# Kernel optimization log

Measured on AMD Instinct MI355X. Metric: run time of the kernel, lower is better.

Reference implementation:

```python
import jax, jax.numpy as jnp
import numpy as np

N_NODES = 20000

def gcn(h, W, b, src, dst):
    # DGL GraphConv, norm='both': D_out^-1/2 on src, aggregate, D_in^-1/2 on dst, then W, b
    E = src.shape[0]
    ones = jnp.ones((E,), dtype=h.dtype)
    out_deg = jnp.clip(jax.ops.segment_sum(ones, src, N_NODES), 1.0)
    in_deg = jnp.clip(jax.ops.segment_sum(ones, dst, N_NODES), 1.0)
    dn_src = jax.lax.rsqrt(out_deg)  # [N]
    dn_dst = jax.lax.rsqrt(in_deg)
    hs = h * dn_src[None, :, None]           # [B,N,H]
    msg = hs[:, src, :]                      # [B,E,H] gather
    agg = jax.vmap(lambda m: jax.ops.segment_sum(m, dst, N_NODES))(msg)  # [B,N,H]
    agg = agg * dn_dst[None, :, None]
    return agg @ W + b

def setup_inputs() -> dict:
    key = jax.random.key(0)
    ks = jax.random.split(key, 16)
    B, N, H, I, E = 4, N_NODES, 128, 64, 320000
    inp = {
        'x': jax.random.normal(ks[0], (B, I), jnp.float32),
        'h_prev': jax.random.normal(ks[1], (B, N, H), jnp.float32),
        'c_prev': jax.random.normal(ks[2], (B, N, H), jnp.float32),
        'src': jax.random.randint(ks[3], (E,), 0, N, jnp.int32),
        'dst': jax.random.randint(ks[4], (E,), 0, N, jnp.int32),
    }
    s_in = 1.0 / np.sqrt(I)
    s_h = 1.0 / np.sqrt(H)
    inp['Wi'] = jax.random.uniform(ks[5], (I, H), jnp.float32, -s_in, s_in)
    inp['bi'] = jax.random.uniform(ks[6], (H,), jnp.float32, -s_in, s_in)
    inp['Wf'] = jax.random.uniform(ks[7], (I, H), jnp.float32, -s_in, s_in)
    inp['bf'] = jax.random.uniform(ks[8], (H,), jnp.float32, -s_in, s_in)
    inp['Wo'] = jax.random.uniform(ks[9], (I, H), jnp.float32, -s_in, s_in)
    inp['bo'] = jax.random.uniform(ks[10], (H,), jnp.float32, -s_in, s_in)
    inp['Wc'] = jax.random.uniform(ks[11], (I, H), jnp.float32, -s_in, s_in)
    inp['bc'] = jax.random.uniform(ks[12], (H,), jnp.float32, -s_in, s_in)
    inp['Wg'] = jax.random.uniform(ks[13], (H, H), jnp.float32, -s_h, s_h)
    inp['bg'] = jax.random.uniform(ks[14], (H,), jnp.float32, -s_h, s_h)
    return inp

def reference(x, h_prev, c_prev, src, dst, Wi, bi, Wf, bf, Wo, bo, Wc, bc, Wg, bg):
    # gcn_h(g, h_prev) is identical in all four gates -> compute once
    gh = gcn(h_prev, Wg, bg, src, dst)  # [B,N,H]
    i_t = jax.nn.sigmoid((x @ Wi + bi)[:, None, :] + gh)
    f_t = jax.nn.sigmoid((x @ Wf + bf)[:, None, :] + gh)
    o_t = jax.nn.sigmoid((x @ Wo + bo)[:, None, :] + gh)
    c_tilde = jnp.tanh((x @ Wc + bc)[:, None, :] + gh)
    c_t = f_t * c_prev + i_t * c_tilde
    h_t = o_t * jnp.tanh(c_t)
    return h_t, c_t
```

## Files before the change

kernel.cpp:

```cpp
#include <hip/hip_runtime.h>
#include <hip/hip_bf16.h>

#define N_NODES 20000
#define B 4
#define H 128
#define I_DIM 64
#define E_MAX 320000
#define CAP 64

typedef __attribute__((ext_vector_type(8))) short short8;
typedef __attribute__((ext_vector_type(4))) float float4v;

__device__ int   g_cnt_dst[N_NODES];
__device__ int   g_deg_src[N_NODES];
__device__ int   g_csr[N_NODES * CAP];
__device__ __align__(16) float g_xg[4 * B * H];
__device__ __align__(16) uint2 g_hs[N_NODES * H];
__device__ __align__(16) unsigned short g_wgB[H * H];

__global__ __launch_bounds__(256)
void degree_kernel(const int* __restrict__ src, int E, int eb,
                   const float* __restrict__ x,
                   const float* __restrict__ Wi, const float* __restrict__ bi,
                   const float* __restrict__ Wf, const float* __restrict__ bf_,
                   const float* __restrict__ Wo, const float* __restrict__ bo,
                   const float* __restrict__ Wc, const float* __restrict__ bc,
                   const float* __restrict__ Wg) {
    int blk = blockIdx.x;
    int t = threadIdx.x;
    if (blk < eb) {
        int e = blk * 256 + t;
        if (e < E) atomicAdd(&g_deg_src[src[e]], 1);
    } else if (blk < eb + 8) {
        int bid = blk - eb;
        int g = bid >> 1;
        int b = ((bid & 1) << 1) | (t >> 7);
        int h = t & 127;
        const float* W;
        const float* bb;
        switch (g) {
            case 0: W = Wi; bb = bi; break;
            case 1: W = Wf; bb = bf_; break;
            case 2: W = Wo; bb = bo; break;
            default: W = Wc; bb = bc; break;
        }
        float acc = bb[h];
#pragma unroll
        for (int i = 0; i < I_DIM; i++)
            acc += x[b * I_DIM + i] * W[i * H + h];
        g_xg[(b * H + h) * 4 + g] = acc;
    } else {
        int i = (blk - eb - 8) * 256 + t;
        int tn = i >> 11;
        int rem = i & 2047;
        int kb = rem >> 9;
        int rem2 = rem & 511;
        int lane = rem2 >> 3;
        int j = rem2 & 7;
        int k  = kb * 32 + (lane >> 4) * 8 + j;
        int nn = tn * 16 + (lane & 15);
        __hip_bfloat16 hv = __float2bfloat16(Wg[k * H + nn]);
        g_wgB[i] = *reinterpret_cast<unsigned short*>(&hv);
    }
}

__global__ __launch_bounds__(256)
void mid_kernel(const float* __restrict__ h_prev,
                const int* __restrict__ src, const int* __restrict__ dst, int E) {
    const int PACK_BLKS = (N_NODES * H) / 256;
    int blk = blockIdx.x;
    int t = threadIdx.x;

    if (blk < PACK_BLKS) {
        int i = blk * 256 + t;
        int n = i >> 7;
        float sc = rsqrtf(fmaxf((float)g_deg_src[n], 1.0f));
        const long stride = (long)N_NODES * H;
        float v0 = h_prev[i] * sc;
        float v1 = h_prev[i + stride] * sc;
        float v2 = h_prev[i + 2 * stride] * sc;
        float v3 = h_prev[i + 3 * stride] * sc;
        __hip_bfloat162 p01 = __float22bfloat162_rn(make_float2(v0, v1));
        __hip_bfloat162 p23 = __float22bfloat162_rn(make_float2(v2, v3));
        uint2 wv;
        wv.x = *reinterpret_cast<unsigned int*>(&p01);
        wv.y = *reinterpret_cast<unsigned int*>(&p23);
        g_hs[i] = wv;
    } else {
        int e = (blk - PACK_BLKS) * 256 + t;
        if (e < E) {
            int d = dst[e];
            int slot = atomicAdd(&g_cnt_dst[d], 1);
            if (slot < CAP) g_csr[(d << 6) + slot] = src[e];
        }
    }
}

__device__ __forceinline__ float fast_sigmoid(float z) {
    return 1.f / (1.f + __expf(-z));
}
__device__ __forceinline__ float fast_tanh(float z) {
    return 1.f - 2.f / (__expf(2.f * z) + 1.f);
}
__device__ __forceinline__ unsigned pack2bf(float lo, float hi) {
    __hip_bfloat162 p = __float22bfloat162_rn(make_float2(lo, hi));
    return *reinterpret_cast<unsigned*>(&p);
}

__global__ __launch_bounds__(256)
void fused_kernel(const float* __restrict__ bg,
                  const float* __restrict__ c_prev,
                  float* __restrict__ out_h, float* __restrict__ out_c) {
    int t = threadIdx.x;
    int w = t >> 6;
    int lane = t & 63;
    int q = (blockIdx.x * 4 + w) * 4;
    const long stride = (long)N_NODES * H;

    __shared__ int            sbase[4][4 * 64];
    __shared__ unsigned short Atile[4][16][136];

    int cnt0 = g_cnt_dst[q + 0];
    int cnt1 = g_cnt_dst[q + 1];
    int cnt2 = g_cnt_dst[q + 2];
    int cnt3 = g_cnt_dst[q + 3];
    float dd0 = rsqrtf(fmaxf((float)cnt0, 1.0f)); if (cnt0 > CAP) cnt0 = CAP;
    float dd1 = rsqrtf(fmaxf((float)cnt1, 1.0f)); if (cnt1 > CAP) cnt1 = CAP;
    float dd2 = rsqrtf(fmaxf((float)cnt2, 1.0f)); if (cnt2 > CAP) cnt2 = CAP;
    float dd3 = rsqrtf(fmaxf((float)cnt3, 1.0f)); if (cnt3 > CAP) cnt3 = CAP;

    {
        int s0 = g_csr[((q + 0) << 6) + (lane < cnt0 ? lane : 0)];
        int s1 = g_csr[((q + 1) << 6) + (lane < cnt1 ? lane : 0)];
        int s2 = g_csr[((q + 2) << 6) + (lane < cnt2 ? lane : 0)];
        int s3 = g_csr[((q + 3) << 6) + (lane < cnt3 ? lane : 0)];
        sbase[w][0 * 64 + lane] = s0 << 6;
        sbase[w][1 * 64 + lane] = s1 << 6;
        sbase[w][2 * 64 + lane] = s2 << 6;
        sbase[w][3 * 64 + lane] = s3 << 6;
    }

    const uint4* hs4 = reinterpret_cast<const uint4*>(g_hs);
    const int* sb = sbase[w];

#define ACCV(v) { \
        __hip_bfloat162 p; float2 f; \
        p = *reinterpret_cast<__hip_bfloat162*>(&(v).x); f = __bfloat1622float2(p); a0 += f.x; a1 += f.y; \
        p = *reinterpret_cast<__hip_bfloat162*>(&(v).y); f = __bfloat1622float2(p); a2 += f.x; a3 += f.y; \
        p = *reinterpret_cast<__hip_bfloat162*>(&(v).z); f = __bfloat1622float2(p); a4 += f.x; a5 += f.y; \
        p = *reinterpret_cast<__hip_bfloat162*>(&(v).w); f = __bfloat1622float2(p); a6 += f.x; a7 += f.y; }

#define GATHER_NODE(i, cnt, dd) { \
        float a0 = 0.f, a1 = 0.f, a2 = 0.f, a3 = 0.f; \
        float a4 = 0.f, a5 = 0.f, a6 = 0.f, a7 = 0.f; \
        int j = 0; \
        for (; j + 16 <= (cnt); j += 16) { \
            int b0 = sb[(i) * 64 + j];      int b1 = sb[(i) * 64 + j + 1]; \
            int b2 = sb[(i) * 64 + j + 2];  int b3 = sb[(i) * 64 + j + 3]; \
            int b4 = sb[(i) * 64 + j + 4];  int b5 = sb[(i) * 64 + j + 5]; \
            int b6 = sb[(i) * 64 + j + 6];  int b7 = sb[(i) * 64 + j + 7]; \
            int b8 = sb[(i) * 64 + j + 8];  int b9 = sb[(i) * 64 + j + 9]; \
            int b10 = sb[(i) * 64 + j + 10]; int b11 = sb[(i) * 64 + j + 11]; \
            int b12 = sb[(i) * 64 + j + 12]; int b13 = sb[(i) * 64 + j + 13]; \
            int b14 = sb[(i) * 64 + j + 14]; int b15 = sb[(i) * 64 + j + 15]; \
            uint4 v0 = hs4[b0 + lane];   uint4 v1 = hs4[b1 + lane]; \
            uint4 v2 = hs4[b2 + lane];   uint4 v3 = hs4[b3 + lane]; \
            uint4 v4 = hs4[b4 + lane];   uint4 v5 = hs4[b5 + lane]; \
            uint4 v6 = hs4[b6 + lane];   uint4 v7 = hs4[b7 + lane]; \
            uint4 v8 = hs4[b8 + lane];   uint4 v9 = hs4[b9 + lane]; \
            uint4 v10 = hs4[b10 + lane]; uint4 v11 = hs4[b11 + lane]; \
            uint4 v12 = hs4[b12 + lane]; uint4 v13 = hs4[b13 + lane]; \
            uint4 v14 = hs4[b14 + lane]; uint4 v15 = hs4[b15 + lane]; \
            ACCV(v0);  ACCV(v1);  ACCV(v2);  ACCV(v3); \
            ACCV(v4);  ACCV(v5);  ACCV(v6);  ACCV(v7); \
            ACCV(v8);  ACCV(v9);  ACCV(v10); ACCV(v11); \
            ACCV(v12); ACCV(v13); ACCV(v14); ACCV(v15); \
        } \
        for (; j + 4 <= (cnt); j += 4) { \
            int b0 = sb[(i) * 64 + j];     int b1 = sb[(i) * 64 + j + 1]; \
            int b2 = sb[(i) * 64 + j + 2]; int b3 = sb[(i) * 64 + j + 3]; \
            uint4 v0 = hs4[b0 + lane]; uint4 v1 = hs4[b1 + lane]; \
            uint4 v2 = hs4[b2 + lane]; uint4 v3 = hs4[b3 + lane]; \
            ACCV(v0); ACCV(v1); ACCV(v2); ACCV(v3); \
        } \
        for (; j < (cnt); j++) { \
            uint4 v = hs4[sb[(i) * 64 + j] + lane]; \
            ACCV(v); \
        } \
        *reinterpret_cast<unsigned*>(&Atile[w][(i) * 4 + 0][2 * lane]) = pack2bf(a0 * (dd), a4 * (dd)); \
        *reinterpret_cast<unsigned*>(&Atile[w][(i) * 4 + 1][2 * lane]) = pack2bf(a1 * (dd), a5 * (dd)); \
        *reinterpret_cast<unsigned*>(&Atile[w][(i) * 4 + 2][2 * lane]) = pack2bf(a2 * (dd), a6 * (dd)); \
        *reinterpret_cast<unsigned*>(&Atile[w][(i) * 4 + 3][2 * lane]) = pack2bf(a3 * (dd), a7 * (dd)); \
    }

    GATHER_NODE(0, cnt0, dd0);
    GATHER_NODE(1, cnt1, dd1);

    int hl = lane & 15;
    long ne = (long)(q + (lane >> 4));
    float cpr[8][4];
#pragma unroll
    for (int tn = 0; tn < 8; tn++) {
        int h = tn * 16 + hl;
#pragma unroll
        for (int jj = 0; jj < 4; jj++)
            cpr[tn][jj] = __builtin_nontemporal_load(
                &c_prev[(long)jj * stride + ne * H + h]);
    }

    GATHER_NODE(2, cnt2, dd2);
    GATHER_NODE(3, cnt3, dd3);
#undef GATHER_NODE
#undef ACCV

    int arow = lane & 15;
    int agrp = lane >> 4;
    float4v c[8];
#pragma unroll
    for (int tn = 0; tn < 8; tn++) c[tn] = (float4v){0.f, 0.f, 0.f, 0.f};
#pragma unroll
    for (int kb = 0; kb < 4; kb++) {
        short8 af = *reinterpret_cast<const short8*>(&Atile[w][arow][kb * 32 + agrp * 8]);
#pragma unroll
        for (int tn = 0; tn < 8; tn++) {
            short8 bf = *reinterpret_cast<const short8*>(
                &g_wgB[((tn * 4 + kb) * 64 + lane) * 8]);
            c[tn] = __builtin_amdgcn_mfma_f32_16x16x32_bf16(af, bf, c[tn], 0, 0, 0);
        }
    }

    const float4* xg4 = reinterpret_cast<const float4*>(g_xg);
#pragma unroll
    for (int tn = 0; tn < 8; tn++) {
        int h = tn * 16 + hl;
        float bgh = bg[h];
#pragma unroll
        for (int jj = 0; jj < 4; jj++) {
            float gh = c[tn][jj] + bgh;
            float4 xv = xg4[jj * H + h];

            float it = fast_sigmoid(xv.x + gh);
            float ft = fast_sigmoid(xv.y + gh);
            float ot = fast_sigmoid(xv.z + gh);
            float ct = fast_tanh(xv.w + gh);

            float cc = ft * cpr[tn][jj] + it * ct;
            float ho = ot * fast_tanh(cc);

            long idx = (long)jj * stride + ne * H + h;
            __builtin_nontemporal_store(ho, &out_h[idx]);
            __builtin_nontemporal_store(cc, &out_c[idx]);
        }
    }

    if (lane < 4) {
        g_cnt_dst[q + lane] = 0;
        g_deg_src[q + lane] = 0;
    }
}

extern "C" void kernel_launch(void* const* d_in, const int* in_sizes, int n_in,
                              void* d_out, int out_size, void* d_ws, size_t ws_size,
                              hipStream_t stream) {
    const float* x      = (const float*)d_in[0];
    const float* h_prev = (const float*)d_in[1];
    const float* c_prev = (const float*)d_in[2];
    const int* src = (const int*)d_in[3];
    const int* dst = (const int*)d_in[4];
    const float* Wi = (const float*)d_in[5];
    const float* bi = (const float*)d_in[6];
    const float* Wf = (const float*)d_in[7];
    const float* bf_ = (const float*)d_in[8];
    const float* Wo = (const float*)d_in[9];
    const float* bo = (const float*)d_in[10];
    const float* Wc = (const float*)d_in[11];
    const float* bc = (const float*)d_in[12];
    const float* Wg = (const float*)d_in[13];
    const float* bg = (const float*)d_in[14];

    int E = in_sizes[3];
    if (E > E_MAX) E = E_MAX;
    int eb = (E + 255) / 256;
    const int PACK_BLKS = (N_NODES * H) / 256;

    degree_kernel<<<eb + 8 + 64, 256, 0, stream>>>(src, E, eb,
        x, Wi, bi, Wf, bf_, Wo, bo, Wc, bc, Wg);
    mid_kernel<<<PACK_BLKS + eb, 256, 0, stream>>>(h_prev, src, dst, E);

    float* out_h = (float*)d_out;
    float* out_c = out_h + (long)B * N_NODES * H;
    fused_kernel<<<N_NODES / 16, 256, 0, stream>>>(bg, c_prev, out_h, out_c);
}
```

Before: 279.6 us.

## Halve nodes per wave in fused GCN-LSTM kernel to double grid size

Each wave now gathers and processes 2 destination nodes instead of 4, and the grid doubles to N/8 blocks. The MFMA tile runs half-filled (rows 8-15 zeroed), and only half the lanes do the gate epilogue. The epilogue is split into two halves to lower accumulator register pressure, and the gather unroll drops from 16 to 8. This trades more parallelism and occupancy for wasted MFMA work and idle lanes in the epilogue.

```diff
diff --git a/kernel.cpp b/kernel.cpp
--- a/kernel.cpp
+++ b/kernel.cpp
@@ -114,30 +114,22 @@
     int t = threadIdx.x;
     int w = t >> 6;
     int lane = t & 63;
-    int q = (blockIdx.x * 4 + w) * 4;
+    int q0 = (blockIdx.x * 4 + w) * 2;
     const long stride = (long)N_NODES * H;
 
-    __shared__ int            sbase[4][4 * 64];
+    __shared__ int            sbase[4][2 * 64];
     __shared__ unsigned short Atile[4][16][136];
 
-    int cnt0 = g_cnt_dst[q + 0];
-    int cnt1 = g_cnt_dst[q + 1];
-    int cnt2 = g_cnt_dst[q + 2];
-    int cnt3 = g_cnt_dst[q + 3];
+    int cnt0 = g_cnt_dst[q0];
+    int cnt1 = g_cnt_dst[q0 + 1];
     float dd0 = rsqrtf(fmaxf((float)cnt0, 1.0f)); if (cnt0 > CAP) cnt0 = CAP;
     float dd1 = rsqrtf(fmaxf((float)cnt1, 1.0f)); if (cnt1 > CAP) cnt1 = CAP;
-    float dd2 = rsqrtf(fmaxf((float)cnt2, 1.0f)); if (cnt2 > CAP) cnt2 = CAP;
-    float dd3 = rsqrtf(fmaxf((float)cnt3, 1.0f)); if (cnt3 > CAP) cnt3 = CAP;
 
     {
-        int s0 = g_csr[((q + 0) << 6) + (lane < cnt0 ? lane : 0)];
-        int s1 = g_csr[((q + 1) << 6) + (lane < cnt1 ? lane : 0)];
-        int s2 = g_csr[((q + 2) << 6) + (lane < cnt2 ? lane : 0)];
-        int s3 = g_csr[((q + 3) << 6) + (lane < cnt3 ? lane : 0)];
-        sbase[w][0 * 64 + lane] = s0 << 6;
-        sbase[w][1 * 64 + lane] = s1 << 6;
-        sbase[w][2 * 64 + lane] = s2 << 6;
-        sbase[w][3 * 64 + lane] = s3 << 6;
+        int s0 = g_csr[(q0 << 6) + (lane < cnt0 ? lane : 0)];
+        int s1 = g_csr[((q0 + 1) << 6) + (lane < cnt1 ? lane : 0)];
+        sbase[w][lane]      = s0 << 6;
+        sbase[w][64 + lane] = s1 << 6;
     }
 
     const uint4* hs4 = reinterpret_cast<const uint4*>(g_hs);
@@ -154,27 +146,17 @@
         float a0 = 0.f, a1 = 0.f, a2 = 0.f, a3 = 0.f; \
         float a4 = 0.f, a5 = 0.f, a6 = 0.f, a7 = 0.f; \
         int j = 0; \
-        for (; j + 16 <= (cnt); j += 16) { \
-            int b0 = sb[(i) * 64 + j];      int b1 = sb[(i) * 64 + j + 1]; \
-            int b2 = sb[(i) * 64 + j + 2];  int b3 = sb[(i) * 64 + j + 3]; \
-            int b4 = sb[(i) * 64 + j + 4];  int b5 = sb[(i) * 64 + j + 5]; \
-            int b6 = sb[(i) * 64 + j + 6];  int b7 = sb[(i) * 64 + j + 7]; \
-            int b8 = sb[(i) * 64 + j + 8];  int b9 = sb[(i) * 64 + j + 9]; \
-            int b10 = sb[(i) * 64 + j + 10]; int b11 = sb[(i) * 64 + j + 11]; \
-            int b12 = sb[(i) * 64 + j + 12]; int b13 = sb[(i) * 64 + j + 13]; \
-            int b14 = sb[(i) * 64 + j + 14]; int b15 = sb[(i) * 64 + j + 15]; \
-            uint4 v0 = hs4[b0 + lane];   uint4 v1 = hs4[b1 + lane]; \
-            uint4 v2 = hs4[b2 + lane];   uint4 v3 = hs4[b3 + lane]; \
-            uint4 v4 = hs4[b4 + lane];   uint4 v5 = hs4[b5 + lane]; \
-            uint4 v6 = hs4[b6 + lane];   uint4 v7 = hs4[b7 + lane]; \
-            uint4 v8 = hs4[b8 + lane];   uint4 v9 = hs4[b9 + lane]; \
-            uint4 v10 = hs4[b10 + lane]; uint4 v11 = hs4[b11 + lane]; \
-            uint4 v12 = hs4[b12 + lane]; uint4 v13 = hs4[b13 + lane]; \
-            uint4 v14 = hs4[b14 + lane]; uint4 v15 = hs4[b15 + lane]; \
-            ACCV(v0);  ACCV(v1);  ACCV(v2);  ACCV(v3); \
-            ACCV(v4);  ACCV(v5);  ACCV(v6);  ACCV(v7); \
-            ACCV(v8);  ACCV(v9);  ACCV(v10); ACCV(v11); \
-            ACCV(v12); ACCV(v13); ACCV(v14); ACCV(v15); \
+        for (; j + 8 <= (cnt); j += 8) { \
+            int b0 = sb[(i) * 64 + j];     int b1 = sb[(i) * 64 + j + 1]; \
+            int b2 = sb[(i) * 64 + j + 2]; int b3 = sb[(i) * 64 + j + 3]; \
+            int b4 = sb[(i) * 64 + j + 4]; int b5 = sb[(i) * 64 + j + 5]; \
+            int b6 = sb[(i) * 64 + j + 6]; int b7 = sb[(i) * 64 + j + 7]; \
+            uint4 v0 = hs4[b0 + lane]; uint4 v1 = hs4[b1 + lane]; \
+            uint4 v2 = hs4[b2 + lane]; uint4 v3 = hs4[b3 + lane]; \
+            uint4 v4 = hs4[b4 + lane]; uint4 v5 = hs4[b5 + lane]; \
+            uint4 v6 = hs4[b6 + lane]; uint4 v7 = hs4[b7 + lane]; \
+            ACCV(v0); ACCV(v1); ACCV(v2); ACCV(v3); \
+            ACCV(v4); ACCV(v5); ACCV(v6); ACCV(v7); \
         } \
         for (; j + 4 <= (cnt); j += 4) { \
             int b0 = sb[(i) * 64 + j];     int b1 = sb[(i) * 64 + j + 1]; \
@@ -195,67 +177,66 @@
 
     GATHER_NODE(0, cnt0, dd0);
     GATHER_NODE(1, cnt1, dd1);
-
-    int hl = lane & 15;
-    long ne = (long)(q + (lane >> 4));
-    float cpr[8][4];
-#pragma unroll
-    for (int tn = 0; tn < 8; tn++) {
-        int h = tn * 16 + hl;
-#pragma unroll
-        for (int jj = 0; jj < 4; jj++)
-            cpr[tn][jj] = __builtin_nontemporal_load(
-                &c_prev[(long)jj * stride + ne * H + h]);
-    }
-
-    GATHER_NODE(2, cnt2, dd2);
-    GATHER_NODE(3, cnt3, dd3);
 #undef GATHER_NODE
 #undef ACCV
 
     int arow = lane & 15;
     int agrp = lane >> 4;
-    float4v c[8];
-#pragma unroll
-    for (int tn = 0; tn < 8; tn++) c[tn] = (float4v){0.f, 0.f, 0.f, 0.f};
-#pragma unroll
-    for (int kb = 0; kb < 4; kb++) {
-        short8 af = *reinterpret_cast<const short8*>(&Atile[w][arow][kb * 32 + agrp * 8]);
-#pragma unroll
-        for (int tn = 0; tn < 8; tn++) {
-            short8 bf = *reinterpret_cast<const short8*>(
-                &g_wgB[((tn * 4 + kb) * 64 + lane) * 8]);
-            c[tn] = __builtin_amdgcn_mfma_f32_16x16x32_bf16(af, bf, c[tn], 0, 0, 0);
-        }
-    }
-
+    int hl = lane & 15;
+    bool act = (lane < 32);
+    long ne = (long)(q0 + (lane >> 4));
     const float4* xg4 = reinterpret_cast<const float4*>(g_xg);
-#pragma unroll
-    for (int tn = 0; tn < 8; tn++) {
-        int h = tn * 16 + hl;
-        float bgh = bg[h];
-#pragma unroll
-        for (int jj = 0; jj < 4; jj++) {
-            float gh = c[tn][jj] + bgh;
-            float4 xv = xg4[jj * H + h];
-
-            float it = fast_sigmoid(xv.x + gh);
-            float ft = fast_sigmoid(xv.y + gh);
-            float ot = fast_sigmoid(xv.z + gh);
-            float ct = fast_tanh(xv.w + gh);
-
-            float cc = ft * cpr[tn][jj] + it * ct;
-            float ho = ot * fast_tanh(cc);
-
-            long idx = (long)jj * stride + ne * H + h;
-            __builtin_nontemporal_store(ho, &out_h[idx]);
-            __builtin_nontemporal_store(cc, &out_c[idx]);
-        }
-    }
-
-    if (lane < 4) {
-        g_cnt_dst[q + lane] = 0;
-        g_deg_src[q + lane] = 0;
+    const short8 zero8 = {0, 0, 0, 0, 0, 0, 0, 0};
+
+#pragma unroll
+    for (int half = 0; half < 2; half++) {
+        float4v c[4];
+#pragma unroll
+        for (int i = 0; i < 4; i++) c[i] = (float4v){0.f, 0.f, 0.f, 0.f};
+#pragma unroll
+        for (int kb = 0; kb < 4; kb++) {
+            short8 af = zero8;
+            if (arow < 8)
+                af = *reinterpret_cast<const short8*>(
+                    &Atile[w][arow][kb * 32 + agrp * 8]);
+#pragma unroll
+            for (int tnn = 0; tnn < 4; tnn++) {
+                int tn = half * 4 + tnn;
+                short8 bf = *reinterpret_cast<const short8*>(
+                    &g_wgB[((tn * 4 + kb) * 64 + lane) * 8]);
+                c[tnn] = __builtin_amdgcn_mfma_f32_16x16x32_bf16(af, bf, c[tnn], 0, 0, 0);
+            }
+        }
+        if (act) {
+#pragma unroll
+            for (int tnn = 0; tnn < 4; tnn++) {
+                int h = (half * 4 + tnn) * 16 + hl;
+                float bgh = bg[h];
+#pragma unroll
+                for (int jj = 0; jj < 4; jj++) {
+                    long idx = (long)jj * stride + ne * H + h;
+                    float cpv = __builtin_nontemporal_load(&c_prev[idx]);
+                    float gh = c[tnn][jj] + bgh;
+                    float4 xv = xg4[jj * H + h];
+
+                    float it = fast_sigmoid(xv.x + gh);
+                    float ft = fast_sigmoid(xv.y + gh);
+                    float ot = fast_sigmoid(xv.z + gh);
+                    float ct = fast_tanh(xv.w + gh);
+
+                    float cc = ft * cpv + it * ct;
+                    float ho = ot * fast_tanh(cc);
+
+                    __builtin_nontemporal_store(ho, &out_h[idx]);
+                    __builtin_nontemporal_store(cc, &out_c[idx]);
+                }
+            }
+        }
+    }
+
+    if (lane < 2) {
+        g_cnt_dst[q0 + lane] = 0;
+        g_deg_src[q0 + lane] = 0;
     }
 }
 
@@ -289,5 +270,5 @@
 
     float* out_h = (float*)d_out;
     float* out_c = out_h + (long)B * N_NODES * H;
-    fused_kernel<<<N_NODES / 16, 256, 0, stream>>>(bg, c_prev, out_h, out_c);
-}
+    fused_kernel<<<N_NODES / 8, 256, 0, stream>>>(bg, c_prev, out_h, out_c);
+}
```

After: 299.5 us. +7.1%, slower.
